# Kernel tuning notes

Hardware: AMD Instinct MI355X
Metric: run time of the kernel (lower is better)

## Reference

```python
import jax, jax.numpy as jnp
import numpy as np

B, C, H, W = 2, 256, 32, 32
PK, CK = 256, 256


def setup_inputs() -> dict:
    key = jax.random.key(0)
    ks = jax.random.split(key, 9)
    s = 1.0 / np.sqrt(C)
    return {
        'x': jax.random.normal(ks[0], (B, C, H, W), jnp.float32),
        'primary_indices': jax.random.randint(ks[1], (B, PK), 0, B * H * W),
        'compare_indices': jax.random.randint(ks[2], (B, CK), 0, B * H * W),
        'pre_w': jax.random.uniform(ks[3], (3, C, C), jnp.float32, -s, s),
        'pre_b': jax.random.uniform(ks[4], (3, C), jnp.float32, -s, s),
        'post_w': jax.random.uniform(ks[5], (2, C, C), jnp.float32, -s, s),
        'post_b': jax.random.uniform(ks[6], (2, C), jnp.float32, -s, s),
        'post_out_w': jax.random.uniform(ks[7], (2, C), jnp.float32, -s, s),
        'post_out_b': jax.random.uniform(ks[8], (2,), jnp.float32, -s, s),
    }


def reference(x, primary_indices, compare_indices, pre_w, pre_b,
              post_w, post_b, post_out_w, post_out_b):
    # pre_compare: stack of 1x1 convs (c->c->c->c), ReLU between layers
    h = x
    for i in range(3):
        h = jnp.einsum('bchw,oc->bohw', h, pre_w[i]) + pre_b[i][None, :, None, None]
        if i < 2:
            h = jax.nn.relu(h)
    bs, c, hh, ww = h.shape
    # flatten to [bs*h*w, c] node features (matches torch transpose+reshape)
    flat = h.reshape(bs, c, hh * ww).transpose(0, 2, 1).reshape(bs * hh * ww, c)
    # gather primary / compare node features with global flat indices
    xp = flat[primary_indices.reshape(-1)].reshape(bs, -1, c).transpose(0, 2, 1)  # [b,c,pk]
    xc = flat[compare_indices.reshape(-1)].reshape(bs, -1, c).transpose(0, 2, 1)  # [b,c,ck]
    # broadcast pairwise squared difference -> [b,c,pk,ck]
    xx = (xp[:, :, :, None] - xc[:, :, None, :]) ** 2
    # post_compare: 1x1 conv stack c->c->c->2, ReLU between layers
    g = xx
    for i in range(2):
        g = jax.nn.relu(jnp.einsum('bcpq,oc->bopq', g, post_w[i]) + post_b[i][None, :, None, None])
    out = jnp.einsum('bcpq,oc->bopq', g, post_out_w) + post_out_b[None, :, None, None]
    return out  # [b, 2, pk, ck]
```

## Files before the change

kernel.cpp:

```cpp
#include <hip/hip_runtime.h>

typedef unsigned short u16;
typedef short bf16x8 __attribute__((ext_vector_type(8)));
typedef float f32x4 __attribute__((ext_vector_type(4)));
typedef u16 u16x4 __attribute__((ext_vector_type(4)));

__device__ __forceinline__ float b2f(u16 h) {
  unsigned u = ((unsigned)h) << 16;
  return __builtin_bit_cast(float, u);
}
__device__ __forceinline__ u16 f2b(float f) {
  unsigned u = __builtin_bit_cast(unsigned, f);
  u = u + 0x7fffu + ((u >> 16) & 1u);
  return (u16)(u >> 16);
}

#if defined(__has_builtin)
#if __has_builtin(__builtin_amdgcn_cvt_pk_bf16_f32)
#define HAVE_CVT_PK_BF16 1
#endif
#endif

__device__ __forceinline__ unsigned f2b_pk(float a, float b) {
#ifdef HAVE_CVT_PK_BF16
  auto v = __builtin_amdgcn_cvt_pk_bf16_f32(a, b);
  unsigned r;
  __builtin_memcpy(&r, &v, 4);
  return r;
#else
  return (unsigned)f2b(a) | (((unsigned)f2b(b)) << 16);
#endif
}
__device__ __forceinline__ bf16x8 pack8(const float* v) {
  union { unsigned u[4]; bf16x8 o; } r;
  r.u[0] = f2b_pk(v[0], v[1]);
  r.u[1] = f2b_pk(v[2], v[3]);
  r.u[2] = f2b_pk(v[4], v[5]);
  r.u[3] = f2b_pk(v[6], v[7]);
  return r.o;
}
__device__ __forceinline__ u16x4 pack4(float a, float b, float c, float d) {
  union { unsigned u[2]; u16x4 o; } r;
  r.u[0] = f2b_pk(a, b);
  r.u[1] = f2b_pk(c, d);
  return r.o;
}
__device__ __forceinline__ void gld_lds16(const void* g, void* l) {
  __builtin_amdgcn_global_load_lds(
      (__attribute__((address_space(1))) void*)(g),
      (__attribute__((address_space(3))) void*)(l), 16, 0, 0);
}

__global__ void dense_edge_prep(const float* __restrict__ x,
                                const float* __restrict__ pre_w,
                                const float* __restrict__ post_w,
                                u16* __restrict__ wb, u16* __restrict__ xt) {
  const int blk = blockIdx.x;
  const int t = threadIdx.x;
  if (blk < 160) {
    const int id = blk * 256 + t;
    const int layer = id >> 13;
    const int sid = id & 8191;
    const int m = sid >> 5;
    const int s8 = sid & 31;
    const float* src = (layer < 2) ? (post_w + layer * 65536)
                                   : (pre_w + (layer - 2) * 65536);
    u16* dst = wb + layer * 65536;
    f32x4 a = *(const f32x4*)(src + m * 256 + s8 * 8);
    f32x4 c = *(const f32x4*)(src + m * 256 + s8 * 8 + 4);
    float tmp[8] = {a[0], a[1], a[2], a[3], c[0], c[1], c[2], c[3]};
    *(bf16x8*)(dst + (s8 * 256 + m) * 8) = pack8(tmp);
  } else {
    __shared__ float tile[32 * 65];
    const int xb = blk - 160;
    const int b = xb >> 7;
    const int ct = (xb >> 4) & 7;
    const int ht = xb & 15;
    const int c0 = ct * 32, hw0 = ht * 64;
#pragma unroll
    for (int rep = 0; rep < 8; rep++) {
      const int idx = rep * 256 + t;
      const int cl = idx >> 6, hl = idx & 63;
      tile[cl * 65 + hl] = x[(b * 256 + c0 + cl) * 1024 + hw0 + hl];
    }
    __syncthreads();
    const int hl = t >> 2, c8 = t & 3;
    float tmp[8];
#pragma unroll
    for (int i = 0; i < 8; i++) tmp[i] = tile[(c8 * 8 + i) * 65 + hl];
    *(bf16x8*)(xt + (b * 1024 + hw0 + hl) * 256 + c0 + c8 * 8) = pack8(tmp);
  }
}

__global__ __launch_bounds__(256, 2) void dense_edge_pre(
    const u16* __restrict__ xt, const u16* __restrict__ wpre,
    const float* __restrict__ preb, u16* __restrict__ flat) {
  __shared__ u16 feat[2][4096];
  const int t = threadIdx.x;
  const int wv = t >> 6, ln = t & 63;
  const int nb = blockIdx.x * 16;
  const int q4 = ln >> 4, r15 = ln & 15;

#pragma unroll
  for (int i = 0; i < 2; i++) {
    const int slot = wv * 128 + i * 64 + ln;
    const int s8 = slot >> 4, nl = slot & 15;
    gld_lds16(xt + (nb + nl) * 256 + s8 * 8, &feat[0][slot * 8]);
  }
  __syncthreads();

#pragma unroll
  for (int l = 0; l < 3; l++) {
    const u16* wl = wpre + l * 65536;
    f32x4 acc[4];
    f32x4 zero = {0.f, 0.f, 0.f, 0.f};
#pragma unroll
    for (int mt = 0; mt < 4; mt++) acc[mt] = zero;
#pragma unroll
    for (int s = 0; s < 8; s++) {
      bf16x8 bv = *(const bf16x8*)(&feat[l & 1][((s * 4 + q4) * 16 + r15) * 8]);
#pragma unroll
      for (int mt = 0; mt < 4; mt++) {
        bf16x8 av = *(const bf16x8*)(wl + ((s * 4 + q4) * 256 + wv * 64 + mt * 16 + r15) * 8);
        acc[mt] = __builtin_amdgcn_mfma_f32_16x16x32_bf16(av, bv, acc[mt], 0, 0, 0);
      }
    }
    if (l < 2) {
#pragma unroll
      for (int mt = 0; mt < 4; mt++) {
        const int o = wv * 64 + mt * 16 + q4 * 4;
        f32x4 bb = *(const f32x4*)(preb + l * 256 + o);
        *(u16x4*)(&feat[(l + 1) & 1][((o >> 3) * 16 + r15) * 8 + (o & 7)]) =
            pack4(fmaxf(acc[mt][0] + bb[0], 0.f), fmaxf(acc[mt][1] + bb[1], 0.f),
                  fmaxf(acc[mt][2] + bb[2], 0.f), fmaxf(acc[mt][3] + bb[3], 0.f));
      }
      __syncthreads();
    } else {
#pragma unroll
      for (int mt = 0; mt < 4; mt++) {
        const int o = wv * 64 + mt * 16 + q4 * 4;
        f32x4 bb = *(const f32x4*)(preb + 512 + o);
        *(u16x4*)(flat + (nb + r15) * 256 + o) =
            pack4(acc[mt][0] + bb[0], acc[mt][1] + bb[1],
                  acc[mt][2] + bb[2], acc[mt][3] + bb[3]);
      }
    }
  }
}

__global__ __launch_bounds__(512, 2) void dense_edge_main(
    const u16* __restrict__ flat, const int* __restrict__ pidx,
    const int* __restrict__ cidx, const u16* __restrict__ w1s,
    const u16* __restrict__ w2s, const float* __restrict__ b1,
    const float* __restrict__ b2, const float* __restrict__ w3,
    const float* __restrict__ b3, float* __restrict__ out) {
  __shared__ u16 xxbuf[16384];
  __shared__ u16 t1buf[2][16384];
  __shared__ u16 qrows[2][2048];
  __shared__ float pbuf[4][2][64];

  const int t = threadIdx.x;
  const int wv = t >> 6;
  const int ln = t & 63;
  const int q4 = ln >> 4, r15 = ln & 15;
  const bool prod = wv < 4;
  const int cw = wv & 3;
  const int blk = blockIdx.x;
  const int tile0 = blk * 8;
  const int b = tile0 >> 10;
  const int pt = (tile0 >> 5) & 31;
  const int qt0 = tile0 & 31;
  const int p0 = pt * 8;

  const u16* wsrc = prod ? w1s : w2s;
  bf16x8 af_w[4][8];
#pragma unroll
  for (int s = 0; s < 8; s++)
#pragma unroll
    for (int mt = 0; mt < 4; mt++)
      af_w[mt][s] = *(const bf16x8*)(wsrc + ((s * 4 + q4) * 256 + cw * 64 + mt * 16 + r15) * 8);

  const int pn = pidx[b * 256 + p0 + (ln >> 3)];
  bf16x8 pch[4];
#pragma unroll
  for (int i = 0; i < 4; i++)
    pch[i] = *(const bf16x8*)(flat + pn * 256 + wv * 32 + i * 8);

  if (prod) {
    const int row = 2 * cw + (ln >> 5);
    const int qn = cidx[b * 256 + qt0 * 8 + row];
    const int m = ln & 31;
    gld_lds16(flat + qn * 256 + ((m ^ (row & 7)) * 8),
              (u16*)qrows[0] + cw * 512 + ln * 8);
  }
  __syncthreads();

#pragma unroll 1
  for (int j = 0; j <= 8; j++) {
    if (j < 8) {
      if (prod && j + 1 < 8) {
        const int row = 2 * cw + (ln >> 5);
        const int qn = cidx[b * 256 + (qt0 + j + 1) * 8 + row];
        const int m = ln & 31;
        gld_lds16(flat + qn * 256 + ((m ^ (row & 7)) * 8),
                  (u16*)qrows[(j + 1) & 1] + cw * 512 + ln * 8);
      }
      {
        const int q = ln & 7;
        const u16* qbase = qrows[j & 1] + q * 256;
#pragma unroll
        for (int i = 0; i < 4; i++) {
          const int c = wv * 4 + i;
          bf16x8 qv = *(const bf16x8*)(qbase + ((c ^ q) * 8));
          bf16x8 pv = pch[i];
          float d[8];
#pragma unroll
          for (int jj = 0; jj < 8; jj++) {
            float dv = b2f((u16)pv[jj]) - b2f((u16)qv[jj]);
            d[jj] = dv * dv;
          }
          *(bf16x8*)(xxbuf + (c * 64 + ln) * 8) = pack8(d);
        }
      }
    }
    if (!prod && j >= 2) {
      const int idx = cw * 64 + ln;
      if (idx < 128) {
        const int o3 = idx >> 6;
        const int n = idx & 63;
        float v = b3[o3] + pbuf[0][o3][n] + pbuf[1][o3][n] + pbuf[2][o3][n] + pbuf[3][o3][n];
        out[((b * 2 + o3) * 256 + p0 + (n >> 3)) * 256 + (qt0 + j - 2) * 8 + (n & 7)] = v;
      }
    }
    __syncthreads();

    if (prod) {
      if (j < 8) {
        f32x4 acc[4][4];
        f32x4 zero = {0.f, 0.f, 0.f, 0.f};
#pragma unroll
        for (int mt = 0; mt < 4; mt++)
#pragma unroll
          for (int nt = 0; nt < 4; nt++) acc[mt][nt] = zero;
#pragma unroll
        for (int s = 0; s < 8; s++) {
          bf16x8 bfr[4];
#pragma unroll
          for (int nt = 0; nt < 4; nt++)
            bfr[nt] = *(const bf16x8*)(xxbuf + ((s * 4 + q4) * 64 + nt * 16 + r15) * 8);
#pragma unroll
          for (int mt = 0; mt < 4; mt++)
#pragma unroll
            for (int nt = 0; nt < 4; nt++)
              acc[mt][nt] = __builtin_amdgcn_mfma_f32_16x16x32_bf16(af_w[mt][s], bfr[nt], acc[mt][nt], 0, 0, 0);
        }
        u16* tdst = t1buf[j & 1];
#pragma unroll
        for (int mt = 0; mt < 4; mt++) {
          const int o = cw * 64 + mt * 16 + q4 * 4;
          f32x4 bb = *(const f32x4*)(b1 + o);
#pragma unroll
          for (int nt = 0; nt < 4; nt++) {
            const int nn = nt * 16 + r15;
            *(u16x4*)(tdst + ((o >> 3) * 64 + nn) * 8 + (o & 7)) =
                pack4(fmaxf(acc[mt][nt][0] + bb[0], 0.f),
                      fmaxf(acc[mt][nt][1] + bb[1], 0.f),
                      fmaxf(acc[mt][nt][2] + bb[2], 0.f),
                      fmaxf(acc[mt][nt][3] + bb[3], 0.f));
          }
        }
      }
    } else if (j >= 1) {
      const u16* tsrc = t1buf[(j - 1) & 1];
      f32x4 acc[4][4];
      f32x4 zero = {0.f, 0.f, 0.f, 0.f};
#pragma unroll
      for (int mt = 0; mt < 4; mt++)
#pragma unroll
        for (int nt = 0; nt < 4; nt++) acc[mt][nt] = zero;
#pragma unroll
      for (int s = 0; s < 8; s++) {
        bf16x8 bfr[4];
#pragma unroll
        for (int nt = 0; nt < 4; nt++)
          bfr[nt] = *(const bf16x8*)(tsrc + ((s * 4 + q4) * 64 + nt * 16 + r15) * 8);
#pragma unroll
        for (int mt = 0; mt < 4; mt++)
#pragma unroll
          for (int nt = 0; nt < 4; nt++)
            acc[mt][nt] = __builtin_amdgcn_mfma_f32_16x16x32_bf16(af_w[mt][s], bfr[nt], acc[mt][nt], 0, 0, 0);
      }
      float part[2][4] = {{0.f, 0.f, 0.f, 0.f}, {0.f, 0.f, 0.f, 0.f}};
#pragma unroll
      for (int mt = 0; mt < 4; mt++) {
        const int o = cw * 64 + mt * 16 + q4 * 4;
        f32x4 bb = *(const f32x4*)(b2 + o);
        f32x4 w3a = *(const f32x4*)(w3 + o);
        f32x4 w3b = *(const f32x4*)(w3 + 256 + o);
#pragma unroll
        for (int nt = 0; nt < 4; nt++) {
#pragma unroll
          for (int r = 0; r < 4; r++) {
            float v = fmaxf(acc[mt][nt][r] + bb[r], 0.f);
            part[0][nt] += v * w3a[r];
            part[1][nt] += v * w3b[r];
          }
        }
      }
#pragma unroll
      for (int o3 = 0; o3 < 2; o3++)
#pragma unroll
        for (int nt = 0; nt < 4; nt++) {
          part[o3][nt] += __shfl_xor(part[o3][nt], 16, 64);
          part[o3][nt] += __shfl_xor(part[o3][nt], 32, 64);
        }
      if (q4 == 0) {
#pragma unroll
        for (int o3 = 0; o3 < 2; o3++)
#pragma unroll
          for (int nt = 0; nt < 4; nt++)
            pbuf[cw][o3][nt * 16 + r15] = part[o3][nt];
      }
    }
    __syncthreads();
  }

  if (!prod) {
    const int idx = cw * 64 + ln;
    if (idx < 128) {
      const int o3 = idx >> 6;
      const int n = idx & 63;
      float v = b3[o3] + pbuf[0][o3][n] + pbuf[1][o3][n] + pbuf[2][o3][n] + pbuf[3][o3][n];
      out[((b * 2 + o3) * 256 + p0 + (n >> 3)) * 256 + (qt0 + 7) * 8 + (n & 7)] = v;
    }
  }
}

extern "C" void kernel_launch(void* const* d_in, const int* in_sizes, int n_in,
                              void* d_out, int out_size, void* d_ws, size_t ws_size,
                              hipStream_t stream) {
  (void)in_sizes; (void)n_in; (void)out_size; (void)ws_size;
  const float* x          = (const float*)d_in[0];
  const int*   pidx       = (const int*)d_in[1];
  const int*   cidx       = (const int*)d_in[2];
  const float* pre_w      = (const float*)d_in[3];
  const float* pre_b      = (const float*)d_in[4];
  const float* post_w     = (const float*)d_in[5];
  const float* post_b     = (const float*)d_in[6];
  const float* post_out_w = (const float*)d_in[7];
  const float* post_out_b = (const float*)d_in[8];
  float* out = (float*)d_out;

  u16* ws   = (u16*)d_ws;
  u16* w1s  = ws;
  u16* w2s  = ws + 65536;
  u16* wpre = ws + 131072;
  u16* xt   = ws + 327680;
  u16* flat = ws + 851968;

  dense_edge_prep<<<416, 256, 0, stream>>>(x, pre_w, post_w, ws, xt);
  dense_edge_pre<<<128, 256, 0, stream>>>(xt, wpre, pre_b, flat);
  dense_edge_main<<<256, 512, 0, stream>>>(flat, pidx, cidx, w1s, w2s,
                                           post_b, post_b + 256,
                                           post_out_w, post_out_b, out);
}
```

Measured before the change: 144.8 us.

## Replace warp-specialized pipelined main kernel with one-tile-per-block sequential MLP

The main kernel drops the producer/consumer warp split and the multi-tile double-buffered loop. Each of 2048 blocks now handles a single 8x8 pair tile and runs both post-compare layers sequentially, reloading the second weight matrix into registers in between. This removes the inter-stage barriers and the serial 8-tile loop, and raises the number of blocks for more parallelism. The cost is reloading both full weight matrices per tile, which multiplies weight traffic through the caches.

```diff
diff --git a/kernel.cpp b/kernel.cpp
--- a/kernel.cpp
+++ b/kernel.cpp
@@ -148,191 +148,150 @@
   }
 }
 
-__global__ __launch_bounds__(512, 2) void dense_edge_main(
+__global__ __launch_bounds__(256, 2) void dense_edge_main(
     const u16* __restrict__ flat, const int* __restrict__ pidx,
     const int* __restrict__ cidx, const u16* __restrict__ w1s,
     const u16* __restrict__ w2s, const float* __restrict__ b1,
     const float* __restrict__ b2, const float* __restrict__ w3,
     const float* __restrict__ b3, float* __restrict__ out) {
   __shared__ u16 xxbuf[16384];
-  __shared__ u16 t1buf[2][16384];
-  __shared__ u16 qrows[2][2048];
+  __shared__ u16 t1buf[16384];
   __shared__ float pbuf[4][2][64];
 
   const int t = threadIdx.x;
   const int wv = t >> 6;
   const int ln = t & 63;
   const int q4 = ln >> 4, r15 = ln & 15;
-  const bool prod = wv < 4;
-  const int cw = wv & 3;
   const int blk = blockIdx.x;
-  const int tile0 = blk * 8;
-  const int b = tile0 >> 10;
-  const int pt = (tile0 >> 5) & 31;
-  const int qt0 = tile0 & 31;
-  const int p0 = pt * 8;
-
-  const u16* wsrc = prod ? w1s : w2s;
+  const int b = blk >> 10;
+  const int pt = (blk >> 5) & 31;
+  const int qt = blk & 31;
+  const int p0 = pt * 8, q0 = qt * 8;
+
   bf16x8 af_w[4][8];
 #pragma unroll
   for (int s = 0; s < 8; s++)
 #pragma unroll
     for (int mt = 0; mt < 4; mt++)
-      af_w[mt][s] = *(const bf16x8*)(wsrc + ((s * 4 + q4) * 256 + cw * 64 + mt * 16 + r15) * 8);
-
-  const int pn = pidx[b * 256 + p0 + (ln >> 3)];
-  bf16x8 pch[4];
-#pragma unroll
-  for (int i = 0; i < 4; i++)
-    pch[i] = *(const bf16x8*)(flat + pn * 256 + wv * 32 + i * 8);
-
-  if (prod) {
-    const int row = 2 * cw + (ln >> 5);
-    const int qn = cidx[b * 256 + qt0 * 8 + row];
-    const int m = ln & 31;
-    gld_lds16(flat + qn * 256 + ((m ^ (row & 7)) * 8),
-              (u16*)qrows[0] + cw * 512 + ln * 8);
+      af_w[mt][s] = *(const bf16x8*)(w1s + ((s * 4 + q4) * 256 + wv * 64 + mt * 16 + r15) * 8);
+
+  {
+    const int pn = pidx[b * 256 + p0 + (ln >> 3)];
+    const int qn = cidx[b * 256 + q0 + (ln & 7)];
+    const u16* prow = flat + pn * 256 + wv * 64;
+    const u16* qrow = flat + qn * 256 + wv * 64;
+#pragma unroll
+    for (int i = 0; i < 8; i++) {
+      bf16x8 av = *(const bf16x8*)(prow + i * 8);
+      bf16x8 bv = *(const bf16x8*)(qrow + i * 8);
+      float d[8];
+#pragma unroll
+      for (int jj = 0; jj < 8; jj++) {
+        float dv = b2f((u16)av[jj]) - b2f((u16)bv[jj]);
+        d[jj] = dv * dv;
+      }
+      *(bf16x8*)(xxbuf + ((wv * 8 + i) * 64 + ln) * 8) = pack8(d);
+    }
   }
   __syncthreads();
 
-#pragma unroll 1
-  for (int j = 0; j <= 8; j++) {
-    if (j < 8) {
-      if (prod && j + 1 < 8) {
-        const int row = 2 * cw + (ln >> 5);
-        const int qn = cidx[b * 256 + (qt0 + j + 1) * 8 + row];
-        const int m = ln & 31;
-        gld_lds16(flat + qn * 256 + ((m ^ (row & 7)) * 8),
-                  (u16*)qrows[(j + 1) & 1] + cw * 512 + ln * 8);
-      }
-      {
-        const int q = ln & 7;
-        const u16* qbase = qrows[j & 1] + q * 256;
-#pragma unroll
-        for (int i = 0; i < 4; i++) {
-          const int c = wv * 4 + i;
-          bf16x8 qv = *(const bf16x8*)(qbase + ((c ^ q) * 8));
-          bf16x8 pv = pch[i];
-          float d[8];
-#pragma unroll
-          for (int jj = 0; jj < 8; jj++) {
-            float dv = b2f((u16)pv[jj]) - b2f((u16)qv[jj]);
-            d[jj] = dv * dv;
-          }
-          *(bf16x8*)(xxbuf + (c * 64 + ln) * 8) = pack8(d);
+  f32x4 acc[4][4];
+  {
+    f32x4 zero = {0.f, 0.f, 0.f, 0.f};
+#pragma unroll
+    for (int mt = 0; mt < 4; mt++)
+#pragma unroll
+      for (int nt = 0; nt < 4; nt++) acc[mt][nt] = zero;
+  }
+#pragma unroll
+  for (int s = 0; s < 8; s++) {
+    bf16x8 bfr[4];
+#pragma unroll
+    for (int nt = 0; nt < 4; nt++)
+      bfr[nt] = *(const bf16x8*)(xxbuf + ((s * 4 + q4) * 64 + nt * 16 + r15) * 8);
+#pragma unroll
+    for (int mt = 0; mt < 4; mt++)
+#pragma unroll
+      for (int nt = 0; nt < 4; nt++)
+        acc[mt][nt] = __builtin_amdgcn_mfma_f32_16x16x32_bf16(af_w[mt][s], bfr[nt], acc[mt][nt], 0, 0, 0);
+  }
+
+#pragma unroll
+  for (int mt = 0; mt < 4; mt++) {
+    const int o = wv * 64 + mt * 16 + q4 * 4;
+    f32x4 bb = *(const f32x4*)(b1 + o);
+#pragma unroll
+    for (int nt = 0; nt < 4; nt++) {
+      const int nn = nt * 16 + r15;
+      *(u16x4*)(t1buf + ((o >> 3) * 64 + nn) * 8 + (o & 7)) =
+          pack4(fmaxf(acc[mt][nt][0] + bb[0], 0.f),
+                fmaxf(acc[mt][nt][1] + bb[1], 0.f),
+                fmaxf(acc[mt][nt][2] + bb[2], 0.f),
+                fmaxf(acc[mt][nt][3] + bb[3], 0.f));
+      acc[mt][nt][0] = 0.f; acc[mt][nt][1] = 0.f;
+      acc[mt][nt][2] = 0.f; acc[mt][nt][3] = 0.f;
+    }
+  }
+#pragma unroll
+  for (int s = 0; s < 8; s++)
+#pragma unroll
+    for (int mt = 0; mt < 4; mt++)
+      af_w[mt][s] = *(const bf16x8*)(w2s + ((s * 4 + q4) * 256 + wv * 64 + mt * 16 + r15) * 8);
+  __syncthreads();
+
+#pragma unroll
+  for (int s = 0; s < 8; s++) {
+    bf16x8 bfr[4];
+#pragma unroll
+    for (int nt = 0; nt < 4; nt++)
+      bfr[nt] = *(const bf16x8*)(t1buf + ((s * 4 + q4) * 64 + nt * 16 + r15) * 8);
+#pragma unroll
+    for (int mt = 0; mt < 4; mt++)
+#pragma unroll
+      for (int nt = 0; nt < 4; nt++)
+        acc[mt][nt] = __builtin_amdgcn_mfma_f32_16x16x32_bf16(af_w[mt][s], bfr[nt], acc[mt][nt], 0, 0, 0);
+  }
+
+  {
+    float part[2][4] = {{0.f, 0.f, 0.f, 0.f}, {0.f, 0.f, 0.f, 0.f}};
+#pragma unroll
+    for (int mt = 0; mt < 4; mt++) {
+      const int o = wv * 64 + mt * 16 + q4 * 4;
+      f32x4 bb = *(const f32x4*)(b2 + o);
+      f32x4 w3a = *(const f32x4*)(w3 + o);
+      f32x4 w3b = *(const f32x4*)(w3 + 256 + o);
+#pragma unroll
+      for (int nt = 0; nt < 4; nt++) {
+#pragma unroll
+        for (int r = 0; r < 4; r++) {
+          float v = fmaxf(acc[mt][nt][r] + bb[r], 0.f);
+          part[0][nt] += v * w3a[r];
+          part[1][nt] += v * w3b[r];
         }
       }
     }
-    if (!prod && j >= 2) {
-      const int idx = cw * 64 + ln;
-      if (idx < 128) {
-        const int o3 = idx >> 6;
-        const int n = idx & 63;
-        float v = b3[o3] + pbuf[0][o3][n] + pbuf[1][o3][n] + pbuf[2][o3][n] + pbuf[3][o3][n];
-        out[((b * 2 + o3) * 256 + p0 + (n >> 3)) * 256 + (qt0 + j - 2) * 8 + (n & 7)] = v;
-      }
-    }
-    __syncthreads();
-
-    if (prod) {
-      if (j < 8) {
-        f32x4 acc[4][4];
-        f32x4 zero = {0.f, 0.f, 0.f, 0.f};
-#pragma unroll
-        for (int mt = 0; mt < 4; mt++)
-#pragma unroll
-          for (int nt = 0; nt < 4; nt++) acc[mt][nt] = zero;
-#pragma unroll
-        for (int s = 0; s < 8; s++) {
-          bf16x8 bfr[4];
-#pragma unroll
-          for (int nt = 0; nt < 4; nt++)
-            bfr[nt] = *(const bf16x8*)(xxbuf + ((s * 4 + q4) * 64 + nt * 16 + r15) * 8);
-#pragma unroll
-          for (int mt = 0; mt < 4; mt++)
-#pragma unroll
-            for (int nt = 0; nt < 4; nt++)
-              acc[mt][nt] = __builtin_amdgcn_mfma_f32_16x16x32_bf16(af_w[mt][s], bfr[nt], acc[mt][nt], 0, 0, 0);
-        }
-        u16* tdst = t1buf[j & 1];
-#pragma unroll
-        for (int mt = 0; mt < 4; mt++) {
-          const int o = cw * 64 + mt * 16 + q4 * 4;
-          f32x4 bb = *(const f32x4*)(b1 + o);
-#pragma unroll
-          for (int nt = 0; nt < 4; nt++) {
-            const int nn = nt * 16 + r15;
-            *(u16x4*)(tdst + ((o >> 3) * 64 + nn) * 8 + (o & 7)) =
-                pack4(fmaxf(acc[mt][nt][0] + bb[0], 0.f),
-                      fmaxf(acc[mt][nt][1] + bb[1], 0.f),
-                      fmaxf(acc[mt][nt][2] + bb[2], 0.f),
-                      fmaxf(acc[mt][nt][3] + bb[3], 0.f));
-          }
-        }
-      }
-    } else if (j >= 1) {
-      const u16* tsrc = t1buf[(j - 1) & 1];
-      f32x4 acc[4][4];
-      f32x4 zero = {0.f, 0.f, 0.f, 0.f};
-#pragma unroll
-      for (int mt = 0; mt < 4; mt++)
-#pragma unroll
-        for (int nt = 0; nt < 4; nt++) acc[mt][nt] = zero;
-#pragma unroll
-      for (int s = 0; s < 8; s++) {
-        bf16x8 bfr[4];
+#pragma unroll
+    for (int o3 = 0; o3 < 2; o3++)
+#pragma unroll
+      for (int nt = 0; nt < 4; nt++) {
+        part[o3][nt] += __shfl_xor(part[o3][nt], 16, 64);
+        part[o3][nt] += __shfl_xor(part[o3][nt], 32, 64);
+      }
+    if (q4 == 0) {
+#pragma unroll
+      for (int o3 = 0; o3 < 2; o3++)
 #pragma unroll
         for (int nt = 0; nt < 4; nt++)
-          bfr[nt] = *(const bf16x8*)(tsrc + ((s * 4 + q4) * 64 + nt * 16 + r15) * 8);
-#pragma unroll
-        for (int mt = 0; mt < 4; mt++)
-#pragma unroll
-          for (int nt = 0; nt < 4; nt++)
-            acc[mt][nt] = __builtin_amdgcn_mfma_f32_16x16x32_bf16(af_w[mt][s], bfr[nt], acc[mt][nt], 0, 0, 0);
-      }
-      float part[2][4] = {{0.f, 0.f, 0.f, 0.f}, {0.f, 0.f, 0.f, 0.f}};
-#pragma unroll
-      for (int mt = 0; mt < 4; mt++) {
-        const int o = cw * 64 + mt * 16 + q4 * 4;
-        f32x4 bb = *(const f32x4*)(b2 + o);
-        f32x4 w3a = *(const f32x4*)(w3 + o);
-        f32x4 w3b = *(const f32x4*)(w3 + 256 + o);
-#pragma unroll
-        for (int nt = 0; nt < 4; nt++) {
-#pragma unroll
-          for (int r = 0; r < 4; r++) {
-            float v = fmaxf(acc[mt][nt][r] + bb[r], 0.f);
-            part[0][nt] += v * w3a[r];
-            part[1][nt] += v * w3b[r];
-          }
-        }
-      }
-#pragma unroll
-      for (int o3 = 0; o3 < 2; o3++)
-#pragma unroll
-        for (int nt = 0; nt < 4; nt++) {
-          part[o3][nt] += __shfl_xor(part[o3][nt], 16, 64);
-          part[o3][nt] += __shfl_xor(part[o3][nt], 32, 64);
-        }
-      if (q4 == 0) {
-#pragma unroll
-        for (int o3 = 0; o3 < 2; o3++)
-#pragma unroll
-          for (int nt = 0; nt < 4; nt++)
-            pbuf[cw][o3][nt * 16 + r15] = part[o3][nt];
-      }
-    }
-    __syncthreads();
-  }
-
-  if (!prod) {
-    const int idx = cw * 64 + ln;
-    if (idx < 128) {
-      const int o3 = idx >> 6;
-      const int n = idx & 63;
-      float v = b3[o3] + pbuf[0][o3][n] + pbuf[1][o3][n] + pbuf[2][o3][n] + pbuf[3][o3][n];
-      out[((b * 2 + o3) * 256 + p0 + (n >> 3)) * 256 + (qt0 + 7) * 8 + (n & 7)] = v;
-    }
+          pbuf[wv][o3][nt * 16 + r15] = part[o3][nt];
+    }
+  }
+  __syncthreads();
+
+  if (t < 128) {
+    const int o3 = t >> 6;
+    const int n = t & 63;
+    float v = b3[o3] + pbuf[0][o3][n] + pbuf[1][o3][n] + pbuf[2][o3][n] + pbuf[3][o3][n];
+    out[((b * 2 + o3) * 256 + p0 + (n >> 3)) * 256 + q0 + (n & 7)] = v;
   }
 }
 
@@ -360,7 +319,7 @@
 
   dense_edge_prep<<<416, 256, 0, stream>>>(x, pre_w, post_w, ws, xt);
   dense_edge_pre<<<128, 256, 0, stream>>>(xt, wpre, pre_b, flat);
-  dense_edge_main<<<256, 512, 0, stream>>>(flat, pidx, cidx, w1s, w2s,
-                                           post_b, post_b + 256,
-                                           post_out_w, post_out_b, out);
-}
+  dense_edge_main<<<2048, 256, 0, stream>>>(flat, pidx, cidx, w1s, w2s,
+                                            post_b, post_b + 256,
+                                            post_out_w, post_out_b, out);
+}
```

New measurement: 129.3 us. -10.7%, faster.
